# Optimization experiments

Hardware: AMD Instinct MI355X
Metric: run time of the kernel (lower is better)

## Reference

```python
import jax, jax.numpy as jnp
import numpy as np

B, T, E, D = 64, 512, 1024, 1024  # batch, enc timesteps, enc hidden, dec hidden


def setup_inputs() -> dict:
    key = jax.random.key(0)
    ks = jax.random.split(key, 9)
    s = lambda fan_in: 1.0 / np.sqrt(fan_in)
    return {
        "hidden": jax.random.normal(ks[0], (B, D), jnp.float32),
        "decoder_out": jax.random.normal(ks[1], (B, D), jnp.float32),
        "encoder_states": jax.random.normal(ks[2], (T, B, E), jnp.float32),
        # attn: Linear(D+E -> 2E)
        "Wa": jax.random.uniform(ks[3], (2 * E, D + E), jnp.float32, -s(D + E), s(D + E)),
        "ba": jax.random.uniform(ks[4], (2 * E,), jnp.float32, -s(D + E), s(D + E)),
        # attn2: Linear(2E -> 1)
        "w2": jax.random.uniform(ks[5], (1, 2 * E), jnp.float32, -s(2 * E), s(2 * E)),
        "b2": jax.random.uniform(ks[6], (1,), jnp.float32, -s(2 * E), s(2 * E)),
        # attn_combine: Linear(D+E -> D)
        "Wc": jax.random.uniform(ks[7], (D, D + E), jnp.float32, -s(D + E), s(D + E)),
        "bc": jax.random.uniform(ks[8], (D,), jnp.float32, -s(D + E), s(D + E)),
    }


def reference(hidden, decoder_out, encoder_states, Wa, ba, w2, b2, Wc, bc):
    d = hidden.shape[1]
    # attn(cat(hidden, enc_t)) = hidden @ Wa[:, :D].T + enc_t @ Wa[:, D:].T + ba
    h_proj = hidden @ Wa[:, :d].T + ba                      # [B, 2E]
    e_proj = jnp.einsum('tbe,fe->tbf', encoder_states, Wa[:, d:])  # [T, B, 2E]
    act = jnp.tanh(h_proj[None, :, :] + e_proj)             # [T, B, 2E]
    scores = jnp.einsum('tbf,f->bt', act, w2[0]) + b2[0]    # [B, T]
    weights = jax.nn.softmax(scores, axis=-1)               # softmax over timesteps
    # weighted sum of encoder states: [B, E]
    applied = jnp.einsum('bt,tbe->be', weights, encoder_states)
    combined = jnp.concatenate([decoder_out, applied], axis=1)  # [B, D+E]
    out = jnp.tanh(combined @ Wc.T + bc)                    # [B, D]
    return out, applied
```

## Files before the change

### kernel.cpp

```cpp
#include <hip/hip_runtime.h>
#include <hip/hip_bf16.h>

#define BB 64
#define TT 512
#define EE 1024
#define DD 1024
#define BK 64

typedef __attribute__((ext_vector_type(8))) short s16x8;
typedef __attribute__((ext_vector_type(4))) float f32x4;

__device__ __forceinline__ float bf2f(unsigned short u) {
    unsigned int x = ((unsigned int)u) << 16;
    return __builtin_bit_cast(float, x);
}
__device__ __forceinline__ unsigned short f2bf(float f) {
    unsigned int u = __builtin_bit_cast(unsigned int, f);
    u += 0x7FFF + ((u >> 16) & 1);
    return (unsigned short)(u >> 16);
}
__device__ __forceinline__ float tanh_fast(float x) {
    x = fminf(fmaxf(x, -15.f), 15.f);
    float e = __expf(2.f * x);
    return (e - 1.f) / (e + 1.f);
}

__device__ __forceinline__ int tile_slot(int row, int g) {
    return (row >> 4) * 128 + (g >> 2) * 64 + (g & 3) * 16 + (row & 15);
}

__global__ __launch_bounds__(256) void conv_encS_kernel(
    const float* __restrict__ enc, unsigned short* __restrict__ encS)
{
    __shared__ short tileL[1024 * 8];
    const int tm  = blockIdx.x;
    const int tk  = blockIdx.y;
    const int tid = threadIdx.x;

#pragma unroll
    for (int it = 0; it < 4; ++it) {
        int cidx = it * 256 + tid;
        int row  = cidx >> 3;
        int g    = cidx & 7;
        const float* src = enc + (size_t)(tm * 128 + row) * 1024 + tk * 64 + g * 8;
        float4 v0 = ((const float4*)src)[0];
        float4 v1 = ((const float4*)src)[1];
        short c[8];
        c[0] = (short)f2bf(v0.x); c[1] = (short)f2bf(v0.y);
        c[2] = (short)f2bf(v0.z); c[3] = (short)f2bf(v0.w);
        c[4] = (short)f2bf(v1.x); c[5] = (short)f2bf(v1.y);
        c[6] = (short)f2bf(v1.z); c[7] = (short)f2bf(v1.w);
        *(s16x8*)&tileL[tile_slot(row, g) * 8] = *(s16x8*)c;
    }
    __syncthreads();
    unsigned short* dst = encS + ((size_t)tm * 16 + tk) * 8192;
#pragma unroll
    for (int it = 0; it < 4; ++it) {
        int s = it * 256 + tid;
        *(s16x8*)&dst[s * 8] = *(const s16x8*)&tileL[s * 8];
    }
}

__global__ __launch_bounds__(256) void conv_waS_kernel(
    const float* __restrict__ Wa, unsigned short* __restrict__ WaS)
{
    __shared__ short tileL[1024 * 8];
    const int tn  = blockIdx.x;
    const int tk  = blockIdx.y;
    const int tid = threadIdx.x;

#pragma unroll
    for (int it = 0; it < 4; ++it) {
        int cidx = it * 256 + tid;
        int row  = cidx >> 3;
        int g    = cidx & 7;
        const float* src = Wa + (size_t)(tn * 128 + row) * 2048 + 1024 + tk * 64 + g * 8;
        float4 v0 = ((const float4*)src)[0];
        float4 v1 = ((const float4*)src)[1];
        short c[8];
        c[0] = (short)f2bf(v0.x); c[1] = (short)f2bf(v0.y);
        c[2] = (short)f2bf(v0.z); c[3] = (short)f2bf(v0.w);
        c[4] = (short)f2bf(v1.x); c[5] = (short)f2bf(v1.y);
        c[6] = (short)f2bf(v1.z); c[7] = (short)f2bf(v1.w);
        *(s16x8*)&tileL[tile_slot(row, g) * 8] = *(s16x8*)c;
    }
    __syncthreads();
    unsigned short* dst = WaS + ((size_t)tn * 16 + tk) * 8192;
#pragma unroll
    for (int it = 0; it < 4; ++it) {
        int s = it * 256 + tid;
        *(s16x8*)&dst[s * 8] = *(const s16x8*)&tileL[s * 8];
    }
}

__global__ __launch_bounds__(256) void hproj_kernel(
    const float* __restrict__ hidden,
    const float* __restrict__ Wa,
    const float* __restrict__ ba,
    float* __restrict__ hp)
{
    __shared__ float sW[8 * 1024];
    const int tid  = threadIdx.x;
    const int lane = tid & 63;
    const int wave = tid >> 6;
    const int f0   = blockIdx.x * 8;

#pragma unroll
    for (int i = 0; i < 8; ++i) {
        int idx = i * 256 + tid;
        int fi  = idx >> 8;
        int c4  = idx & 255;
        ((float4*)sW)[idx] = *(const float4*)(Wa + (size_t)(f0 + fi) * 2048 + c4 * 4);
    }
    __syncthreads();

    for (int bi = 0; bi < 16; ++bi) {
        int b = wave * 16 + bi;
        float h[16];
#pragma unroll
        for (int j = 0; j < 16; ++j) h[j] = hidden[b * 1024 + lane + 64 * j];
#pragma unroll
        for (int fi = 0; fi < 8; ++fi) {
            float s = 0.f;
#pragma unroll
            for (int j = 0; j < 16; ++j) s += h[j] * sW[fi * 1024 + lane + 64 * j];
#pragma unroll
            for (int m = 32; m; m >>= 1) s += __shfl_xor(s, m);
            if (lane == 0) hp[(f0 + fi) * 64 + b] = s + ba[f0 + fi];
        }
    }
}

__global__ __launch_bounds__(256) void gemm_scores(
    const unsigned short* __restrict__ encS,
    const unsigned short* __restrict__ WaS,
    const float* __restrict__ hp,
    const float* __restrict__ w2,
    float* __restrict__ scores)
{
    __shared__ short sA[128 * BK];
    __shared__ short sB[128 * BK];
    __shared__ float rowAcc[128];

    const int tid  = threadIdx.x;
    const int bm   = blockIdx.x;
    const int bn   = blockIdx.y;
    const int lane = tid & 63;
    const int wave = tid >> 6;
    const int wm   = wave >> 1;
    const int wn   = wave & 1;
    const int c    = lane & 15;
    const int quad = lane >> 4;

    f32x4 acc[4][4];
#pragma unroll
    for (int mi = 0; mi < 4; ++mi)
#pragma unroll
        for (int ni = 0; ni < 4; ++ni)
#pragma unroll
            for (int r = 0; r < 4; ++r) acc[mi][ni][r] = 0.f;

    for (int kt = 0; kt < 16; ++kt) {
        const unsigned short* at = encS + ((size_t)bm * 16 + kt) * 8192;
        const unsigned short* bt = WaS  + ((size_t)bn * 16 + kt) * 8192;
#pragma unroll
        for (int i = 0; i < 4; ++i) {
            int s = i * 256 + tid;
            __builtin_amdgcn_global_load_lds(
                (const __attribute__((address_space(1))) void*)(at + s * 8),
                (__attribute__((address_space(3))) void*)&sA[s * 8], 16, 0, 0);
            __builtin_amdgcn_global_load_lds(
                (const __attribute__((address_space(1))) void*)(bt + s * 8),
                (__attribute__((address_space(3))) void*)&sB[s * 8], 16, 0, 0);
        }
        __builtin_amdgcn_s_waitcnt(0);
        __syncthreads();

#pragma unroll
        for (int kk = 0; kk < 2; ++kk) {
            s16x8 aF[4], bF[4];
#pragma unroll
            for (int mi = 0; mi < 4; ++mi)
                aF[mi] = *(const s16x8*)&sA[((wm * 4 + mi) * 128 + kk * 64 + lane) * 8];
#pragma unroll
            for (int ni = 0; ni < 4; ++ni)
                bF[ni] = *(const s16x8*)&sB[((wn * 4 + ni) * 128 + kk * 64 + lane) * 8];

#pragma unroll
            for (int mi = 0; mi < 4; ++mi)
#pragma unroll
                for (int ni = 0; ni < 4; ++ni)
                    acc[mi][ni] = __builtin_amdgcn_mfma_f32_16x16x32_bf16(
                        aF[mi], bF[ni], acc[mi][ni], 0, 0, 0);
        }
        __syncthreads();
    }

    float w2v[4];
#pragma unroll
    for (int ni = 0; ni < 4; ++ni) w2v[ni] = w2[bn * 128 + wn * 64 + ni * 16 + c];

    if (tid < 128) rowAcc[tid] = 0.f;
    __syncthreads();

#pragma unroll
    for (int mi = 0; mi < 4; ++mi) {
        int lrow0 = wm * 64 + mi * 16 + quad * 4;
        int b0    = (bm * 128 + lrow0) & 63;
        f32x4 hp4[4];
#pragma unroll
        for (int ni = 0; ni < 4; ++ni)
            hp4[ni] = *(const f32x4*)&hp[(bn * 128 + wn * 64 + ni * 16 + c) * 64 + b0];
#pragma unroll
        for (int r = 0; r < 4; ++r) {
            float s = 0.f;
#pragma unroll
            for (int ni = 0; ni < 4; ++ni)
                s += tanh_fast(acc[mi][ni][r] + hp4[ni][r]) * w2v[ni];
            s += __shfl_xor(s, 1);
            s += __shfl_xor(s, 2);
            s += __shfl_xor(s, 4);
            s += __shfl_xor(s, 8);
            if (c == 0) atomicAdd(&rowAcc[lrow0 + r], s);
        }
    }
    __syncthreads();
    if (tid < 128) {
        int grow = bm * 128 + tid;
        int b = grow & 63;
        int t = grow >> 6;
        atomicAdd(&scores[b * TT + t], rowAcc[tid]);
    }
}

__global__ __launch_bounds__(256) void softmax_kernel(float* __restrict__ scores)
{
    __shared__ float wmax[4];
    __shared__ float wsum[4];
    const int b   = blockIdx.x;
    const int tid = threadIdx.x;
    float* row = scores + b * TT;

    float v0 = row[tid], v1 = row[tid + 256];
    float m = fmaxf(v0, v1);
#pragma unroll
    for (int s = 32; s; s >>= 1) m = fmaxf(m, __shfl_xor(m, s));
    if ((tid & 63) == 0) wmax[tid >> 6] = m;
    __syncthreads();
    m = fmaxf(fmaxf(wmax[0], wmax[1]), fmaxf(wmax[2], wmax[3]));

    float e0 = __expf(v0 - m), e1 = __expf(v1 - m);
    float s = e0 + e1;
#pragma unroll
    for (int t = 32; t; t >>= 1) s += __shfl_xor(s, t);
    if ((tid & 63) == 0) wsum[tid >> 6] = s;
    __syncthreads();
    float inv = 1.f / (wsum[0] + wsum[1] + wsum[2] + wsum[3]);
    row[tid]       = e0 * inv;
    row[tid + 256] = e1 * inv;
}

__global__ __launch_bounds__(256) void applied_part_kernel(
    const float* __restrict__ enc,
    const float* __restrict__ w,
    float* __restrict__ part)
{
    __shared__ float red[128 * 8];
    const int tc  = blockIdx.x;
    const int b   = blockIdx.y;
    const int tid = threadIdx.x;
    const int eo  = tid & 127;
    const int th  = tid >> 7;
    const int e0  = eo * 8;

    float a[8];
#pragma unroll
    for (int j = 0; j < 8; ++j) a[j] = 0.f;

    for (int it = 0; it < 16; ++it) {
        int t = tc * 32 + th * 16 + it;
        float wt = w[b * TT + t];
        const float* src = enc + ((size_t)(t * BB + b)) * EE + e0;
        float4 v0 = ((const float4*)src)[0];
        float4 v1 = ((const float4*)src)[1];
        a[0] += wt * v0.x; a[1] += wt * v0.y; a[2] += wt * v0.z; a[3] += wt * v0.w;
        a[4] += wt * v1.x; a[5] += wt * v1.y; a[6] += wt * v1.z; a[7] += wt * v1.w;
    }
    if (th == 1) {
#pragma unroll
        for (int j = 0; j < 8; ++j) red[eo * 8 + j] = a[j];
    }
    __syncthreads();
    if (th == 0) {
        float* dst = part + ((size_t)tc * 64 + b) * 1024 + e0;
#pragma unroll
        for (int j = 0; j < 8; ++j) dst[j] = a[j] + red[eo * 8 + j];
    }
}

__global__ __launch_bounds__(256) void applied_reduce_kernel(
    const float* __restrict__ part, float* __restrict__ out_applied)
{
    int idx = blockIdx.x * 256 + threadIdx.x;
    float s = 0.f;
#pragma unroll
    for (int tc = 0; tc < 16; ++tc) s += part[tc * 65536 + idx];
    out_applied[idx] = s;
}

__global__ __launch_bounds__(256) void combine_kernel(
    const float* __restrict__ dec,
    const float* applied,
    const float* __restrict__ Wc,
    const float* __restrict__ bc,
    float* out0)
{
    const int g    = blockIdx.x * 4 + (threadIdx.x >> 6);
    const int lane = threadIdx.x & 63;
    const int d    = g >> 6;
    const int b    = g & 63;

    const float4* wc4 = (const float4*)Wc + (size_t)d * 512;
    const float4* de4 = (const float4*)dec + (size_t)b * 256;
    const float4* ap4 = (const float4*)applied + (size_t)b * 256;

    float s = 0.f;
#pragma unroll
    for (int j = 0; j < 4; ++j) {
        float4 a = de4[j * 64 + lane];
        float4 wv = wc4[j * 64 + lane];
        s += a.x * wv.x + a.y * wv.y + a.z * wv.z + a.w * wv.w;
    }
#pragma unroll
    for (int j = 0; j < 4; ++j) {
        float4 a = ap4[j * 64 + lane];
        float4 wv = wc4[256 + j * 64 + lane];
        s += a.x * wv.x + a.y * wv.y + a.z * wv.z + a.w * wv.w;
    }
#pragma unroll
    for (int m = 32; m; m >>= 1) s += __shfl_xor(s, m);
    if (lane == 0) out0[b * DD + d] = tanh_fast(s + bc[d]);
}

extern "C" void kernel_launch(void* const* d_in, const int* in_sizes, int n_in,
                              void* d_out, int out_size, void* d_ws, size_t ws_size,
                              hipStream_t stream) {
    const float* hidden = (const float*)d_in[0];
    const float* dec    = (const float*)d_in[1];
    const float* enc    = (const float*)d_in[2];
    const float* Wa     = (const float*)d_in[3];
    const float* ba     = (const float*)d_in[4];
    const float* w2     = (const float*)d_in[5];
    const float* Wc     = (const float*)d_in[7];
    const float* bc     = (const float*)d_in[8];
    float* out = (float*)d_out;

    unsigned short* encS = (unsigned short*)d_ws;
    unsigned short* WaS  = encS + (size_t)33554432;
    float* hp     = (float*)(WaS + (size_t)2097152);
    float* scores = hp + 131072;
    float* part   = scores + 32768;

    hipMemsetAsync(scores, 0, BB * TT * sizeof(float), stream);
    dim3 gc(256, 16);
    conv_encS_kernel<<<gc, 256, 0, stream>>>(enc, encS);
    dim3 gw(16, 16);
    conv_waS_kernel<<<gw, 256, 0, stream>>>(Wa, WaS);
    hproj_kernel<<<256, 256, 0, stream>>>(hidden, Wa, ba, hp);
    dim3 g2(256, 16);
    gemm_scores<<<g2, 256, 0, stream>>>(encS, WaS, hp, w2, scores);
    softmax_kernel<<<BB, 256, 0, stream>>>(scores);
    dim3 g3(16, 64);
    applied_part_kernel<<<g3, 256, 0, stream>>>(enc, scores, part);
    applied_reduce_kernel<<<256, 256, 0, stream>>>(part, out + BB * DD);
    combine_kernel<<<16384, 256, 0, stream>>>(dec, out + BB * DD, Wc, bc, out);
}
```

Baseline: 548.8 us.

## Double-buffer LDS tiles in score GEMM and remap blocks across XCDs

The scores GEMM now prefetches the next K tile into a second LDS buffer while MFMAs consume the current one. This is meant to hide global-to-LDS load latency behind compute. It also replaces the 2D grid with a 1D grid whose block index is permuted so neighbouring tiles land on the same XCD, improving L2 reuse. MFMA sections are wrapped in s_setprio, and the explicit vmcnt wait is dropped, so the code relies on __syncthreads to order the async LDS loads; LDS use doubles, which may reduce occupancy.

```diff
diff --git a/kernel.cpp b/kernel.cpp
--- a/kernel.cpp
+++ b/kernel.cpp
@@ -138,13 +138,15 @@
     const float* __restrict__ w2,
     float* __restrict__ scores)
 {
-    __shared__ short sA[128 * BK];
-    __shared__ short sB[128 * BK];
+    __shared__ short sA[2][128 * BK];
+    __shared__ short sB[2][128 * BK];
     __shared__ float rowAcc[128];
 
     const int tid  = threadIdx.x;
-    const int bm   = blockIdx.x;
-    const int bn   = blockIdx.y;
+    const int bid  = blockIdx.x;
+    const int w    = (bid & 7) * 512 + (bid >> 3);
+    const int bm   = w >> 4;
+    const int bn   = w & 15;
     const int lane = tid & 63;
     const int wave = tid >> 6;
     const int wm   = wave >> 1;
@@ -160,38 +162,49 @@
 #pragma unroll
             for (int r = 0; r < 4; ++r) acc[mi][ni][r] = 0.f;
 
-    for (int kt = 0; kt < 16; ++kt) {
-        const unsigned short* at = encS + ((size_t)bm * 16 + kt) * 8192;
-        const unsigned short* bt = WaS  + ((size_t)bn * 16 + kt) * 8192;
+    const unsigned short* atBase = encS + (size_t)bm * 16 * 8192;
+    const unsigned short* btBase = WaS  + (size_t)bn * 16 * 8192;
+
+    auto STAGE = [&](int kt, int buf) {
+        const unsigned short* at = atBase + (size_t)kt * 8192;
+        const unsigned short* bt = btBase + (size_t)kt * 8192;
 #pragma unroll
         for (int i = 0; i < 4; ++i) {
             int s = i * 256 + tid;
             __builtin_amdgcn_global_load_lds(
                 (const __attribute__((address_space(1))) void*)(at + s * 8),
-                (__attribute__((address_space(3))) void*)&sA[s * 8], 16, 0, 0);
+                (__attribute__((address_space(3))) void*)&sA[buf][s * 8], 16, 0, 0);
             __builtin_amdgcn_global_load_lds(
                 (const __attribute__((address_space(1))) void*)(bt + s * 8),
-                (__attribute__((address_space(3))) void*)&sB[s * 8], 16, 0, 0);
+                (__attribute__((address_space(3))) void*)&sB[buf][s * 8], 16, 0, 0);
         }
-        __builtin_amdgcn_s_waitcnt(0);
-        __syncthreads();
+    };
+
+    STAGE(0, 0);
+    __syncthreads();
+
+    for (int kt = 0; kt < 16; ++kt) {
+        const int cur = kt & 1;
+        if (kt < 15) STAGE(kt + 1, cur ^ 1);
 
 #pragma unroll
         for (int kk = 0; kk < 2; ++kk) {
             s16x8 aF[4], bF[4];
 #pragma unroll
             for (int mi = 0; mi < 4; ++mi)
-                aF[mi] = *(const s16x8*)&sA[((wm * 4 + mi) * 128 + kk * 64 + lane) * 8];
+                aF[mi] = *(const s16x8*)&sA[cur][((wm * 4 + mi) * 128 + kk * 64 + lane) * 8];
 #pragma unroll
             for (int ni = 0; ni < 4; ++ni)
-                bF[ni] = *(const s16x8*)&sB[((wn * 4 + ni) * 128 + kk * 64 + lane) * 8];
-
+                bF[ni] = *(const s16x8*)&sB[cur][((wn * 4 + ni) * 128 + kk * 64 + lane) * 8];
+
+            __builtin_amdgcn_s_setprio(1);
 #pragma unroll
             for (int mi = 0; mi < 4; ++mi)
 #pragma unroll
                 for (int ni = 0; ni < 4; ++ni)
                     acc[mi][ni] = __builtin_amdgcn_mfma_f32_16x16x32_bf16(
                         aF[mi], bF[ni], acc[mi][ni], 0, 0, 0);
+            __builtin_amdgcn_s_setprio(0);
         }
         __syncthreads();
     }
@@ -367,8 +380,7 @@
     dim3 gw(16, 16);
     conv_waS_kernel<<<gw, 256, 0, stream>>>(Wa, WaS);
     hproj_kernel<<<256, 256, 0, stream>>>(hidden, Wa, ba, hp);
-    dim3 g2(256, 16);
-    gemm_scores<<<g2, 256, 0, stream>>>(encS, WaS, hp, w2, scores);
+    gemm_scores<<<4096, 256, 0, stream>>>(encS, WaS, hp, w2, scores);
     softmax_kernel<<<BB, 256, 0, stream>>>(scores);
     dim3 g3(16, 64);
     applied_part_kernel<<<g3, 256, 0, stream>>>(enc, scores, part);
```

New measurement: 548.2 us. Within noise of the previous version (-0.1%).
